# Kernel optimization log

Measured on AMD Instinct MI355X. Metric: run time of the kernel, lower is better.

The kernel has to match this reference:

```python
import jax, jax.numpy as jnp
import numpy as np
from math import factorial
from fractions import Fraction

# irreps: '0e + 1o + 2e + 3o' for in1, in2 and target (mul=1 each, channels separate)
L_IN1 = [0, 1, 2, 3]
L_IN2 = [0, 1, 2, 3]
L_MAX_OUT = 3
NCHANNELS = 64
BATCH = 10000
DIM_IN = sum(2 * l + 1 for l in L_IN1)  # 16


def _su2_cg(j1, m1, j2, m2, j3, m3):
    # Racah formula, exact rational arithmetic (matches e3nn _su2_cg)
    if m3 != m1 + m2 or not (abs(j1 - j2) <= j3 <= j1 + j2):
        return 0.0
    f = factorial
    vmin = max(-j1 + j2 + m3, -j1 + m1, 0)
    vmax = min(j2 + j3 + m1, j3 - j1 + j2, j3 + m3)
    C = (2 * j3 + 1) * Fraction(
        f(j3 + j1 - j2) * f(j3 - j1 + j2) * f(j1 + j2 - j3) * f(j3 + m3) * f(j3 - m3),
        f(j1 + j2 + j3 + 1) * f(j1 - m1) * f(j1 + m1) * f(j2 - m2) * f(j2 + m2))
    S = Fraction(0)
    for v in range(vmin, vmax + 1):
        S += (-1) ** (v + j2 + m2) * Fraction(
            f(j2 + j3 + m1 - v) * f(j1 - m1 + v),
            f(v) * f(j3 - j1 + j2 - v) * f(j3 + m3 - v) * f(v + j1 - j2 - m3))
    return float(C) ** 0.5 * float(S)


def _q_real_to_complex(l):
    # change of basis real SH -> complex SH (matches e3nn, incl. (-i)^l phase)
    q = np.zeros((2 * l + 1, 2 * l + 1), dtype=np.complex128)
    for m in range(-l, 0):
        q[l + m, l + abs(m)] = 1 / np.sqrt(2)
        q[l + m, l - abs(m)] = -1j / np.sqrt(2)
    q[l, l] = 1
    for m in range(1, l + 1):
        q[l + m, l + abs(m)] = (-1) ** m / np.sqrt(2)
        q[l + m, l - abs(m)] = 1j * (-1) ** m / np.sqrt(2)
    return (-1j) ** l * q


def _wigner_3j(l1, l2, l3):
    # real-basis Wigner 3j, unit Frobenius norm (matches e3nn o3.wigner_3j)
    C = np.zeros((2 * l1 + 1, 2 * l2 + 1, 2 * l3 + 1), dtype=np.complex128)
    for m1 in range(-l1, l1 + 1):
        for m2 in range(-l2, l2 + 1):
            for m3 in range(-l3, l3 + 1):
                C[l1 + m1, l2 + m2, l3 + m3] = _su2_cg(l1, m1, l2, m2, l3, m3)
    Q1, Q2, Q3 = _q_real_to_complex(l1), _q_real_to_complex(l2), _q_real_to_complex(l3)
    C = np.einsum('ij,kl,mn,ikn->jlm', Q1, Q2, np.conj(Q3.T), C)
    C = np.real(C)
    return C / np.linalg.norm(C)


def _build_sparse_cg():
    # enumerate instructions exactly as the torch module: i over in1, j over in2,
    # l3 ascending, kept iff parity matches target ((-1)^l3 == (-1)^(l1+l2)) and l3<=3.
    # component normalization, one path per output slot -> path_weight = sqrt(2*l3+1)
    mu1s, mu2s, mu3s, cgs = [], [], [], []
    off3 = 0
    for i, l1 in enumerate(L_IN1):
        off1 = sum(2 * l + 1 for l in L_IN1[:i])
        for j, l2 in enumerate(L_IN2):
            off2 = sum(2 * l + 1 for l in L_IN2[:j])
            for l3 in range(abs(l1 - l2), l1 + l2 + 1):
                if l3 > L_MAX_OUT or (l1 + l2 + l3) % 2 != 0:
                    continue
                cg = _wigner_3j(l1, l2, l3) * np.sqrt(2 * l3 + 1)
                m1, m2, m3 = np.nonzero(np.abs(cg) > 1e-12)
                mu1s.append(m1 + off1)
                mu2s.append(m2 + off2)
                mu3s.append(m3 + off3)
                cgs.append(cg[m1, m2, m3])
                off3 += 2 * l3 + 1
    return (np.concatenate(mu1s).astype(np.int32),
            np.concatenate(mu2s).astype(np.int32),
            np.concatenate(mu3s).astype(np.int32),
            np.concatenate(cgs).astype(np.float32),
            off3)


MU1, MU2, MU3, CG_NP, DIM_OUT = _build_sparse_cg()  # DIM_OUT == 99
CG = jnp.asarray(CG_NP)


def setup_inputs() -> dict:
    key = jax.random.key(0)
    k1, k2 = jax.random.split(key)
    x = jax.random.normal(k1, (BATCH, DIM_IN, NCHANNELS), dtype=jnp.float32)
    y = jax.random.normal(k2, (BATCH, DIM_IN, NCHANNELS), dtype=jnp.float32)
    return {"x": x, "y": y}


def reference(x, y):
    # fused gather-multiply-scatter over all CG nonzeros, vectorized over batch
    g = x[:, MU1, :] * CG[None, :, None] * y[:, MU2, :]  # [B, nnz, C]
    out = jnp.zeros((x.shape[0], DIM_OUT, x.shape[2]), x.dtype).at[:, MU3, :].add(g)
    return out
```

## Files before the change

### kernel.cpp

```cpp
#include <hip/hip_runtime.h>

#define BATCH 10000
#define NCH 64
#define DIM_IN 16
#define DIM_OUT 99

typedef float f32x4 __attribute__((ext_vector_type(4)));

namespace cgc {

struct cx { double re; double im; };

constexpr cx cmul(cx a, cx b) {
    return cx{a.re * b.re - a.im * b.im, a.re * b.im + a.im * b.re};
}

constexpr double cfact(int n) {
    double r = 1.0;
    for (int i = 2; i <= n; ++i) r *= (double)i;
    return r;
}

constexpr double csqrt(double x) {
    if (x <= 0.0) return 0.0;
    double y = x > 1.0 ? x : 1.0;
    for (int i = 0; i < 100; ++i) y = 0.5 * (y + x / y);
    return y;
}

constexpr int imax(int a, int b) { return a > b ? a : b; }
constexpr int imin(int a, int b) { return a < b ? a : b; }
constexpr int iabs(int a) { return a < 0 ? -a : a; }

constexpr double su2_cg(int j1, int m1, int j2, int m2, int j3, int m3) {
    if (m3 != m1 + m2) return 0.0;
    if (j3 < iabs(j1 - j2) || j3 > j1 + j2) return 0.0;
    int vmin = imax(imax(-j1 + j2 + m3, -j1 + m1), 0);
    int vmax = imin(imin(j2 + j3 + m1, j3 - j1 + j2), j3 + m3);
    double C = (2.0 * j3 + 1.0) *
        (cfact(j3 + j1 - j2) * cfact(j3 - j1 + j2) * cfact(j1 + j2 - j3) *
         cfact(j3 + m3) * cfact(j3 - m3)) /
        (cfact(j1 + j2 + j3 + 1) * cfact(j1 - m1) * cfact(j1 + m1) *
         cfact(j2 - m2) * cfact(j2 + m2));
    double S = 0.0;
    for (int v = vmin; v <= vmax; ++v) {
        double t = (cfact(j2 + j3 + m1 - v) * cfact(j1 - m1 + v)) /
                   (cfact(v) * cfact(j3 - j1 + j2 - v) * cfact(j3 + m3 - v) *
                    cfact(v + j1 - j2 - m3));
        S += ((v + j2 + m2) & 1) ? -t : t;
    }
    return csqrt(C) * S;
}

constexpr void fill_q(int l, cx* q) {
    const int n = 2 * l + 1;
    const double is2 = 0.70710678118654752440;
    for (int e = 0; e < n * n; ++e) q[e] = cx{0.0, 0.0};
    for (int m = -l; m < 0; ++m) {
        q[(l + m) * n + (l - m)] = cx{is2, 0.0};
        q[(l + m) * n + (l + m)] = cx{0.0, -is2};
    }
    q[l * n + l] = cx{1.0, 0.0};
    for (int m = 1; m <= l; ++m) {
        double s = (m & 1) ? -1.0 : 1.0;
        q[(l + m) * n + (l + m)] = cx{s * is2, 0.0};
        q[(l + m) * n + (l - m)] = cx{0.0, s * is2};
    }
    cx ph = (l & 3) == 0 ? cx{1.0, 0.0}
          : (l & 3) == 1 ? cx{0.0, -1.0}
          : (l & 3) == 2 ? cx{-1.0, 0.0}
                         : cx{0.0, 1.0};
    for (int e = 0; e < n * n; ++e) q[e] = cmul(ph, q[e]);
}

template<int l1, int l2, int l3>
struct InstCG { float v[(2 * l1 + 1) * (2 * l2 + 1) * (2 * l3 + 1)]; };

template<int l1, int l2, int l3>
constexpr InstCG<l1, l2, l3> make_inst() {
    constexpr int n1 = 2 * l1 + 1, n2 = 2 * l2 + 1, n3 = 2 * l3 + 1;
    double C[n1 * n2 * n3] = {};
    for (int i = 0; i < n1; ++i)
        for (int k = 0; k < n2; ++k)
            for (int nn = 0; nn < n3; ++nn)
                C[(i * n2 + k) * n3 + nn] = su2_cg(l1, i - l1, l2, k - l2, l3, nn - l3);
    cx Q1[n1 * n1] = {}; cx Q2[n2 * n2] = {}; cx Q3[n3 * n3] = {};
    fill_q(l1, Q1); fill_q(l2, Q2); fill_q(l3, Q3);
    double R[n1 * n2 * n3] = {};
    double ss = 0.0;
    for (int j = 0; j < n1; ++j)
        for (int lc = 0; lc < n2; ++lc)
            for (int m = 0; m < n3; ++m) {
                double ar = 0.0;
                for (int i = 0; i < n1; ++i) {
                    cx q1 = Q1[i * n1 + j];
                    if (q1.re == 0.0 && q1.im == 0.0) continue;
                    for (int k = 0; k < n2; ++k) {
                        cx q12 = cmul(q1, Q2[k * n2 + lc]);
                        if (q12.re == 0.0 && q12.im == 0.0) continue;
                        for (int nn = 0; nn < n3; ++nn) {
                            double cc = C[(i * n2 + k) * n3 + nn];
                            if (cc == 0.0) continue;
                            cx q3 = Q3[nn * n3 + m];
                            ar += (q12.re * q3.re + q12.im * q3.im) * cc;
                        }
                    }
                }
                R[(j * n2 + lc) * n3 + m] = ar;
                ss += ar * ar;
            }
    double scale = csqrt((double)n3) / csqrt(ss);
    InstCG<l1, l2, l3> T{};
    for (int e = 0; e < n1 * n2 * n3; ++e) T.v[e] = (float)(R[e] * scale);
    return T;
}

}

template<int l1, int l2, int l3, int o1, int o3>
__device__ __forceinline__ void do_inst(const f32x4* xv, const f32x4* ybl, f32x4* o4) {
    constexpr int n1 = 2 * l1 + 1, n2 = 2 * l2 + 1, n3 = 2 * l3 + 1;
    constexpr cgc::InstCG<l1, l2, l3> T = cgc::make_inst<l1, l2, l3>();
    f32x4 acc[n3];
#pragma unroll
    for (int m3 = 0; m3 < n3; ++m3) acc[m3] = (f32x4)0.0f;
#pragma unroll
    for (int m1 = 0; m1 < n1; ++m1) {
#pragma unroll
        for (int m2 = 0; m2 < n2; ++m2) {
            const f32x4 p = xv[o1 + m1] * ybl[m2];
#pragma unroll
            for (int m3 = 0; m3 < n3; ++m3) {
                const float c = T.v[(m1 * n2 + m2) * n3 + m3];
                if (c != 0.0f) acc[m3] += c * p;
            }
        }
    }
#pragma unroll
    for (int m3 = 0; m3 < n3; ++m3)
        __builtin_nontemporal_store(acc[m3], &o4[(o3 + m3) * 16]);
}

__global__ __launch_bounds__(64, 3) void tp_main(const float* __restrict__ x,
                                                 const float* __restrict__ y,
                                                 float* __restrict__ out) {
    const int g = blockIdx.x * blockDim.x + threadIdx.x;
    const int b = g >> 4;
    const int cl = g & 15;

    const f32x4* x4 = reinterpret_cast<const f32x4*>(x + (size_t)b * (DIM_IN * NCH)) + cl;
    const f32x4* y4 = reinterpret_cast<const f32x4*>(y + (size_t)b * (DIM_IN * NCH)) + cl;
    f32x4* o4 = reinterpret_cast<f32x4*>(out + (size_t)b * (DIM_OUT * NCH)) + cl;

    f32x4 xv[DIM_IN];
#pragma unroll
    for (int i = 0; i < DIM_IN; ++i) xv[i] = __builtin_nontemporal_load(&x4[i * 16]);

    {
        f32x4 ybl[1];
        ybl[0] = __builtin_nontemporal_load(&y4[0 * 16]);
        do_inst<0,0,0, 0,0 >(xv, ybl, o4);
        do_inst<1,0,1, 1,16>(xv, ybl, o4);
        do_inst<2,0,2, 4,40>(xv, ybl, o4);
        do_inst<3,0,3, 9,71>(xv, ybl, o4);
    }
    {
        f32x4 ybl[3];
#pragma unroll
        for (int k = 0; k < 3; ++k) ybl[k] = __builtin_nontemporal_load(&y4[(1 + k) * 16]);
        do_inst<0,1,1, 0,1 >(xv, ybl, o4);
        do_inst<1,1,0, 1,19>(xv, ybl, o4);
        do_inst<1,1,2, 1,20>(xv, ybl, o4);
        do_inst<2,1,1, 4,45>(xv, ybl, o4);
        do_inst<2,1,3, 4,48>(xv, ybl, o4);
        do_inst<3,1,2, 9,78>(xv, ybl, o4);
    }
    {
        f32x4 ybl[5];
#pragma unroll
        for (int k = 0; k < 5; ++k) ybl[k] = __builtin_nontemporal_load(&y4[(4 + k) * 16]);
        do_inst<0,2,2, 0,4 >(xv, ybl, o4);
        do_inst<1,2,1, 1,25>(xv, ybl, o4);
        do_inst<1,2,3, 1,28>(xv, ybl, o4);
        do_inst<2,2,0, 4,55>(xv, ybl, o4);
        do_inst<2,2,2, 4,56>(xv, ybl, o4);
        do_inst<3,2,1, 9,83>(xv, ybl, o4);
        do_inst<3,2,3, 9,86>(xv, ybl, o4);
    }
    {
        f32x4 ybl[7];
#pragma unroll
        for (int k = 0; k < 7; ++k) ybl[k] = __builtin_nontemporal_load(&y4[(9 + k) * 16]);
        do_inst<0,3,3, 0,9 >(xv, ybl, o4);
        do_inst<1,3,2, 1,35>(xv, ybl, o4);
        do_inst<2,3,1, 4,61>(xv, ybl, o4);
        do_inst<2,3,3, 4,64>(xv, ybl, o4);
        do_inst<3,3,0, 9,93>(xv, ybl, o4);
        do_inst<3,3,2, 9,94>(xv, ybl, o4);
    }
}

extern "C" void kernel_launch(void* const* d_in, const int* in_sizes, int n_in,
                              void* d_out, int out_size, void* d_ws, size_t ws_size,
                              hipStream_t stream) {
    const float* x = (const float*)d_in[0];
    const float* y = (const float*)d_in[1];
    float* out = (float*)d_out;
    hipLaunchKernelGGL(tp_main, dim3(BATCH * 16 / 64), dim3(64), 0, stream,
                       x, y, out);
}
```

Baseline: 76.11 us.

## Stage outputs through per-wave LDS ring to emit contiguous row stores

The kernel now keeps y in registers and loops over x blocks, ordering instructions by output slot. Results go into a per-wave shared-memory ring and are flushed in groups of four output rows. The flush is transposed so each 16-lane group writes a full 256-byte row for one batch element, rather than each instruction storing scattered rows. The block size is doubled to 128 and nontemporal loads and stores are dropped. In exchange this adds LDS traffic, relies on wave-synchronous ring reuse with no barriers, and raises register pressure from holding all of y.

```diff
diff --git a/kernel.cpp b/kernel.cpp
--- a/kernel.cpp
+++ b/kernel.cpp
@@ -117,8 +117,9 @@
 
 }
 
-template<int l1, int l2, int l3, int o1, int o3>
-__device__ __forceinline__ void do_inst(const f32x4* xv, const f32x4* ybl, f32x4* o4) {
+template<int l1, int l2, int l3, int o2, int o3>
+__device__ __forceinline__ void do_inst(const f32x4* xbl, const f32x4* yv,
+                                        float* ringw, int lane) {
     constexpr int n1 = 2 * l1 + 1, n2 = 2 * l2 + 1, n3 = 2 * l3 + 1;
     constexpr cgc::InstCG<l1, l2, l3> T = cgc::make_inst<l1, l2, l3>();
     f32x4 acc[n3];
@@ -128,7 +129,7 @@
     for (int m1 = 0; m1 < n1; ++m1) {
 #pragma unroll
         for (int m2 = 0; m2 < n2; ++m2) {
-            const f32x4 p = xv[o1 + m1] * ybl[m2];
+            const f32x4 p = xbl[m1] * yv[o2 + m2];
 #pragma unroll
             for (int m3 = 0; m3 < n3; ++m3) {
                 const float c = T.v[(m1 * n2 + m2) * n3 + m3];
@@ -136,67 +137,123 @@
             }
         }
     }
-#pragma unroll
-    for (int m3 = 0; m3 < n3; ++m3)
-        __builtin_nontemporal_store(acc[m3], &o4[(o3 + m3) * 16]);
-}
-
-__global__ __launch_bounds__(64, 3) void tp_main(const float* __restrict__ x,
-                                                 const float* __restrict__ y,
-                                                 float* __restrict__ out) {
-    const int g = blockIdx.x * blockDim.x + threadIdx.x;
+    const int wbase = ((lane >> 4) << 6) + ((lane & 15) << 2);
+#pragma unroll
+    for (int m3 = 0; m3 < n3; ++m3) {
+        constexpr int dummy = 0; (void)dummy;
+        *reinterpret_cast<f32x4*>(&ringw[(((o3 + m3) & 15) << 8) + wbase]) = acc[m3];
+    }
+}
+
+__device__ __forceinline__ void flush4(const float* ringw, int k, float* __restrict__ out,
+                                       int b0, int lane) {
+    const int sl = 4 * k + (lane >> 4);
+    const int src = ((sl & 15) << 8) + ((lane & 15) << 2);
+#pragma unroll
+    for (int r = 0; r < 4; ++r) {
+        const f32x4 v = *reinterpret_cast<const f32x4*>(&ringw[src + (r << 6)]);
+        *reinterpret_cast<f32x4*>(&out[(size_t)(b0 + r) * (DIM_OUT * NCH)
+                                       + (sl << 6) + ((lane & 15) << 2)]) = v;
+    }
+}
+
+__global__ __launch_bounds__(128, 3) void tp_main(const float* __restrict__ x,
+                                                  const float* __restrict__ y,
+                                                  float* __restrict__ out) {
+    __shared__ float ring[2][16][4][64];
+
+    const int tid = threadIdx.x;
+    const int wid = tid >> 6;
+    const int lane = tid & 63;
+    const int g = blockIdx.x * 128 + tid;
     const int b = g >> 4;
     const int cl = g & 15;
+    const int b0 = b - (lane >> 4);
+
+    float* ringw = &ring[wid][0][0][0];
 
     const f32x4* x4 = reinterpret_cast<const f32x4*>(x + (size_t)b * (DIM_IN * NCH)) + cl;
     const f32x4* y4 = reinterpret_cast<const f32x4*>(y + (size_t)b * (DIM_IN * NCH)) + cl;
-    f32x4* o4 = reinterpret_cast<f32x4*>(out + (size_t)b * (DIM_OUT * NCH)) + cl;
-
-    f32x4 xv[DIM_IN];
-#pragma unroll
-    for (int i = 0; i < DIM_IN; ++i) xv[i] = __builtin_nontemporal_load(&x4[i * 16]);
-
-    {
-        f32x4 ybl[1];
-        ybl[0] = __builtin_nontemporal_load(&y4[0 * 16]);
-        do_inst<0,0,0, 0,0 >(xv, ybl, o4);
-        do_inst<1,0,1, 1,16>(xv, ybl, o4);
-        do_inst<2,0,2, 4,40>(xv, ybl, o4);
-        do_inst<3,0,3, 9,71>(xv, ybl, o4);
-    }
-    {
-        f32x4 ybl[3];
-#pragma unroll
-        for (int k = 0; k < 3; ++k) ybl[k] = __builtin_nontemporal_load(&y4[(1 + k) * 16]);
-        do_inst<0,1,1, 0,1 >(xv, ybl, o4);
-        do_inst<1,1,0, 1,19>(xv, ybl, o4);
-        do_inst<1,1,2, 1,20>(xv, ybl, o4);
-        do_inst<2,1,1, 4,45>(xv, ybl, o4);
-        do_inst<2,1,3, 4,48>(xv, ybl, o4);
-        do_inst<3,1,2, 9,78>(xv, ybl, o4);
-    }
-    {
-        f32x4 ybl[5];
-#pragma unroll
-        for (int k = 0; k < 5; ++k) ybl[k] = __builtin_nontemporal_load(&y4[(4 + k) * 16]);
-        do_inst<0,2,2, 0,4 >(xv, ybl, o4);
-        do_inst<1,2,1, 1,25>(xv, ybl, o4);
-        do_inst<1,2,3, 1,28>(xv, ybl, o4);
-        do_inst<2,2,0, 4,55>(xv, ybl, o4);
-        do_inst<2,2,2, 4,56>(xv, ybl, o4);
-        do_inst<3,2,1, 9,83>(xv, ybl, o4);
-        do_inst<3,2,3, 9,86>(xv, ybl, o4);
-    }
-    {
-        f32x4 ybl[7];
-#pragma unroll
-        for (int k = 0; k < 7; ++k) ybl[k] = __builtin_nontemporal_load(&y4[(9 + k) * 16]);
-        do_inst<0,3,3, 0,9 >(xv, ybl, o4);
-        do_inst<1,3,2, 1,35>(xv, ybl, o4);
-        do_inst<2,3,1, 4,61>(xv, ybl, o4);
-        do_inst<2,3,3, 4,64>(xv, ybl, o4);
-        do_inst<3,3,0, 9,93>(xv, ybl, o4);
-        do_inst<3,3,2, 9,94>(xv, ybl, o4);
+
+    f32x4 yv[DIM_IN];
+#pragma unroll
+    for (int i = 0; i < DIM_IN; ++i) yv[i] = y4[i * 16];
+
+    {
+        f32x4 xbl[1];
+        xbl[0] = x4[0 * 16];
+        do_inst<0,0,0, 0,0>(xbl, yv, ringw, lane);
+        do_inst<0,1,1, 1,1>(xbl, yv, ringw, lane);
+        flush4(ringw, 0, out, b0, lane);
+        do_inst<0,2,2, 4,4>(xbl, yv, ringw, lane);
+        flush4(ringw, 1, out, b0, lane);
+        do_inst<0,3,3, 9,9>(xbl, yv, ringw, lane);
+        flush4(ringw, 2, out, b0, lane);
+        flush4(ringw, 3, out, b0, lane);
+    }
+    {
+        f32x4 xbl[3];
+#pragma unroll
+        for (int i = 0; i < 3; ++i) xbl[i] = x4[(1 + i) * 16];
+        do_inst<1,0,1, 0,16>(xbl, yv, ringw, lane);
+        do_inst<1,1,0, 1,19>(xbl, yv, ringw, lane);
+        flush4(ringw, 4, out, b0, lane);
+        do_inst<1,1,2, 1,20>(xbl, yv, ringw, lane);
+        flush4(ringw, 5, out, b0, lane);
+        do_inst<1,2,1, 4,25>(xbl, yv, ringw, lane);
+        flush4(ringw, 6, out, b0, lane);
+        do_inst<1,2,3, 4,28>(xbl, yv, ringw, lane);
+        flush4(ringw, 7, out, b0, lane);
+        do_inst<1,3,2, 9,35>(xbl, yv, ringw, lane);
+        flush4(ringw, 8, out, b0, lane);
+        flush4(ringw, 9, out, b0, lane);
+    }
+    {
+        f32x4 xbl[5];
+#pragma unroll
+        for (int i = 0; i < 5; ++i) xbl[i] = x4[(4 + i) * 16];
+        do_inst<2,0,2, 0,40>(xbl, yv, ringw, lane);
+        flush4(ringw, 10, out, b0, lane);
+        do_inst<2,1,1, 1,45>(xbl, yv, ringw, lane);
+        flush4(ringw, 11, out, b0, lane);
+        do_inst<2,1,3, 1,48>(xbl, yv, ringw, lane);
+        flush4(ringw, 12, out, b0, lane);
+        do_inst<2,2,0, 4,55>(xbl, yv, ringw, lane);
+        flush4(ringw, 13, out, b0, lane);
+        do_inst<2,2,2, 4,56>(xbl, yv, ringw, lane);
+        flush4(ringw, 14, out, b0, lane);
+        do_inst<2,3,1, 9,61>(xbl, yv, ringw, lane);
+        flush4(ringw, 15, out, b0, lane);
+        do_inst<2,3,3, 9,64>(xbl, yv, ringw, lane);
+        flush4(ringw, 16, out, b0, lane);
+    }
+    {
+        f32x4 xbl[7];
+#pragma unroll
+        for (int i = 0; i < 7; ++i) xbl[i] = x4[(9 + i) * 16];
+        do_inst<3,0,3, 0,71>(xbl, yv, ringw, lane);
+        flush4(ringw, 17, out, b0, lane);
+        flush4(ringw, 18, out, b0, lane);
+        do_inst<3,1,2, 1,78>(xbl, yv, ringw, lane);
+        flush4(ringw, 19, out, b0, lane);
+        do_inst<3,2,1, 4,83>(xbl, yv, ringw, lane);
+        flush4(ringw, 20, out, b0, lane);
+        do_inst<3,2,3, 4,86>(xbl, yv, ringw, lane);
+        flush4(ringw, 21, out, b0, lane);
+        flush4(ringw, 22, out, b0, lane);
+        do_inst<3,3,0, 9,93>(xbl, yv, ringw, lane);
+        do_inst<3,3,2, 9,94>(xbl, yv, ringw, lane);
+        flush4(ringw, 23, out, b0, lane);
+        if (lane < 48) {
+            const int sl = 96 + (lane >> 4);
+            const int src = ((sl & 15) << 8) + ((lane & 15) << 2);
+#pragma unroll
+            for (int r = 0; r < 4; ++r) {
+                const f32x4 v = *reinterpret_cast<const f32x4*>(&ringw[src + (r << 6)]);
+                *reinterpret_cast<f32x4*>(&out[(size_t)(b0 + r) * (DIM_OUT * NCH)
+                                               + (sl << 6) + ((lane & 15) << 2)]) = v;
+            }
+        }
     }
 }
 
@@ -206,6 +263,6 @@
     const float* x = (const float*)d_in[0];
     const float* y = (const float*)d_in[1];
     float* out = (float*)d_out;
-    hipLaunchKernelGGL(tp_main, dim3(BATCH * 16 / 64), dim3(64), 0, stream,
+    hipLaunchKernelGGL(tp_main, dim3(BATCH * 16 / 128), dim3(128), 0, stream,
                        x, y, out);
 }
```

After: 83.25 us. 1.09x slower.
